# Kernel tuning notes

Hardware: AMD Instinct MI355X
Metric: run time of the kernel (lower is better)

The kernel has to match this reference:

```python
import jax, jax.numpy as jnp
import numpy as np

NUM_MOVIES = 100000
MOVIE_FEAT = 128
USER_FEAT = 128
BATCH = 16384
N_NBRS = 50
D0, D1, D2 = 256, 256, 128  # layer_dims


def setup_inputs() -> dict:
    key = jax.random.key(0)
    ks = jax.random.split(key, 16)
    inp = {
        "users": jax.random.normal(ks[0], (BATCH, USER_FEAT), jnp.float32),
        "pos_movies": jax.random.normal(ks[1], (BATCH, MOVIE_FEAT), jnp.float32),
        "neg_movies": jax.random.normal(ks[2], (BATCH, MOVIE_FEAT), jnp.float32),
        "user_ids": jax.random.randint(ks[3], (BATCH,), 0, BATCH),
        "pos_movie_ids": jax.random.randint(ks[4], (BATCH,), 0, NUM_MOVIES),
        "neg_movie_ids": jax.random.randint(ks[5], (BATCH,), 0, NUM_MOVIES),
        "nbr_ids": jax.random.randint(ks[6], (BATCH, N_NBRS), 0, NUM_MOVIES),
        # learned params / buffers
        "movie_table": jax.random.normal(ks[7], (NUM_MOVIES, MOVIE_FEAT), jnp.float32),
        "Wu": jax.random.normal(ks[8], (USER_FEAT, D0), jnp.float32) * (1.0 / np.sqrt(USER_FEAT)),
        "bu": jnp.zeros((D0,), jnp.float32),
        "Wm": jax.random.normal(ks[9], (MOVIE_FEAT, D0), jnp.float32) * (1.0 / np.sqrt(MOVIE_FEAT)),
        "bm": jnp.zeros((D0,), jnp.float32),
        "W1": jax.random.normal(ks[10], (D0, D1), jnp.float32) * (1.0 / np.sqrt(D0)),
        "b1": jnp.zeros((D1,), jnp.float32),
        "W2": jax.random.normal(ks[11], (D1, D2), jnp.float32) * (1.0 / np.sqrt(D1)),
        "b2": jnp.zeros((D2,), jnp.float32),
    }
    return inp


def reference(users, pos_movies, neg_movies, user_ids, pos_movie_ids, neg_movie_ids,
              nbr_ids, movie_table, Wu, bu, Wm, bm, W1, b1, W2, b2):
    # user_projection / movie_projection
    user_emb = users @ Wu + bu                      # [B, D0]
    movie_emb = movie_table @ Wm + bm               # [N, D0]
    pos_emb = movie_emb[pos_movie_ids]              # [B, D0]
    neg_emb = movie_emb[neg_movie_ids]              # [B, D0]
    # vectorized replacement of the per-user neighbor gather + mean loop
    nbr_mean = jnp.mean(movie_emb[nbr_ids], axis=1)  # [B, N_NBRS, D0] -> [B, D0]
    user_emb = user_emb + nbr_mean
    x = jnp.stack([user_emb, pos_emb, neg_emb], axis=0)  # [3, B, D0]
    x = jax.nn.relu(x @ W1 + b1)
    x = jax.nn.relu(x @ W2 + b2)
    return (x[0], x[1], x[2])
```

## Files before the change

kernel.cpp:

```cpp
#include <hip/hip_runtime.h>
#include <hip/hip_bf16.h>

#define BATCH_N   16384
#define FEAT      128
#define NNBR      50
#define NUM_MOVIES_N 100000

typedef short  short8  __attribute__((ext_vector_type(8)));
typedef float  floatx4 __attribute__((ext_vector_type(4)));
typedef unsigned int u32;

__device__ __forceinline__ __hip_bfloat16 f2bf(float x) { return __float2bfloat16(x); }
__device__ __forceinline__ float bfb2f(short s) {
  union { u32 u; float f; } c; c.u = ((u32)(unsigned short)s) << 16; return c.f;
}

__device__ __forceinline__ void gld16(const __hip_bfloat16* g, __hip_bfloat16* l) {
  __builtin_amdgcn_global_load_lds(
      (const __attribute__((address_space(1))) u32*)g,
      (__attribute__((address_space(3))) u32*)l, 16, 0, 0);
}

__device__ __forceinline__ floatx4 mfma16(short8 a, short8 b, floatx4 c) {
  return __builtin_amdgcn_mfma_f32_16x16x32_bf16(a, b, c, 0, 0, 0);
}

#define WAITVM2 asm volatile("s_waitcnt vmcnt(2)" ::: "memory")
#define WAITVM0 asm volatile("s_waitcnt vmcnt(0)" ::: "memory")

#define CONV_BLOCKS (NUM_MOVIES_N * FEAT / (256 * 8))
__global__ __launch_bounds__(256) void prep_all(
    const float* __restrict__ t, __hip_bfloat16* __restrict__ tb,
    const float* __restrict__ Wu, const float* __restrict__ Wm,
    const float* __restrict__ W1, const float* __restrict__ W2,
    const float* __restrict__ bu, const float* __restrict__ bm,
    __hip_bfloat16* __restrict__ WcatT, __hip_bfloat16* __restrict__ WmT,
    __hip_bfloat16* __restrict__ W1T,  __hip_bfloat16* __restrict__ W2T,
    float* __restrict__ bc, unsigned int* __restrict__ ctr) {
  int bid = blockIdx.x;
  if (bid < CONV_BLOCKS) {
    size_t i = ((size_t)bid * 256 + threadIdx.x) * 8;
    float4 v0 = *(const float4*)(t + i);
    float4 v1 = *(const float4*)(t + i + 4);
    __hip_bfloat16 o[8];
    o[0] = f2bf(v0.x); o[1] = f2bf(v0.y); o[2] = f2bf(v0.z); o[3] = f2bf(v0.w);
    o[4] = f2bf(v1.x); o[5] = f2bf(v1.y); o[6] = f2bf(v1.z); o[7] = f2bf(v1.w);
    *(short8*)(tb + i) = *(short8*)o;
  } else {
    int idx = (bid - CONV_BLOCKS) * 256 + threadIdx.x;
    int n = idx & 255, k = idx >> 8;
    float v = (k < 128) ? Wu[k * 256 + n] : Wm[(k - 128) * 256 + n];
    WcatT[n * 256 + k] = f2bf(v);
    W1T[n * 256 + k]   = f2bf(W1[k * 256 + n]);
    if (k < 128) WmT[n * 128 + k] = f2bf(Wm[k * 256 + n]);
    if (idx < 32768) {
      int k2 = idx >> 7, n2 = idx & 127;
      W2T[n2 * 256 + k2] = f2bf(W2[k2 * 128 + n2]);
    }
    if (idx < 256) bc[idx] = bu[idx] + bm[idx];
    if (idx == 0) *ctr = 0;
  }
}

template <int K0, int NCOL, bool RELU, bool TOGLB>
__device__ __forceinline__ void layer(
    const __hip_bfloat16* Ain,
    const __hip_bfloat16* __restrict__ Wt, const float* __restrict__ bias,
    __hip_bfloat16* Olds, float* __restrict__ Oglb,
    int wid, int quad, int lrow) {
  constexpr int KK = K0 / 32;
  constexpr int JN = NCOL / 128;
  const int c0 = wid * JN * 16;

  short8 bfr[JN][KK];
  float  bv[JN];
  #pragma unroll
  for (int j = 0; j < JN; ++j) {
    #pragma unroll
    for (int kc = 0; kc < KK; ++kc)
      bfr[j][kc] = *(const short8*)(Wt + (size_t)(c0 + j * 16 + lrow) * K0 +
                                    kc * 32 + quad * 8);
    bv[j] = bias[c0 + j * 16 + lrow];
  }

  #pragma unroll
  for (int it = 0; it < 4; ++it) {
    int r = it * 16 + lrow;
    short8 af[KK];
    #pragma unroll
    for (int kc = 0; kc < KK; ++kc)
      af[kc] = *(const short8*)&Ain[r * K0 + (((kc * 4 + quad) ^ (r & 7)) << 3)];
    floatx4 pa[JN], pb[JN];
    #pragma unroll
    for (int j = 0; j < JN; ++j) { pa[j] = {}; pb[j] = {}; }
    #pragma unroll
    for (int kc = 0; kc < KK; kc += 2)
      #pragma unroll
      for (int j = 0; j < JN; ++j) {
        pa[j] = mfma16(af[kc],     bfr[j][kc],     pa[j]);
        pb[j] = mfma16(af[kc + 1], bfr[j][kc + 1], pb[j]);
      }
    #pragma unroll
    for (int j = 0; j < JN; ++j) {
      floatx4 a = pa[j] + pb[j];
      int col = c0 + j * 16 + lrow;
      #pragma unroll
      for (int rr = 0; rr < 4; ++rr) {
        int row = it * 16 + quad * 4 + rr;
        float v = a[rr] + bv[j];
        if (RELU) v = fmaxf(v, 0.f);
        if (TOGLB) {
          Oglb[(size_t)row * NCOL + col] = v;
        } else {
          int ch = col >> 3;
          Olds[row * 256 + (((ch ^ (row & 7)) << 3) | (col & 7))] = f2bf(v);
        }
      }
    }
  }
}

__global__ __launch_bounds__(512)
__attribute__((amdgpu_waves_per_eu(2, 2)))
void fused_mlp(
    const float* __restrict__ users,
    const __hip_bfloat16* __restrict__ tb,
    const int* __restrict__ pos_ids, const int* __restrict__ neg_ids,
    const int* __restrict__ nbr_ids,
    const __hip_bfloat16* __restrict__ WcatT,
    const __hip_bfloat16* __restrict__ WmT,
    const __hip_bfloat16* __restrict__ W1T,
    const __hip_bfloat16* __restrict__ W2T,
    const float* __restrict__ bc, const float* __restrict__ bmv,
    const float* __restrict__ b1, const float* __restrict__ b2,
    __hip_bfloat16* __restrict__ A_user, unsigned int* __restrict__ ctr,
    float* __restrict__ out) {
  __shared__ __hip_bfloat16 A_lds[64 * 256];
  __shared__ __hip_bfloat16 E_lds[64 * 256];

  const int t    = threadIdx.x;
  const int lane = t & 63, wid = t >> 6;
  const int quad = lane >> 4, lrow = lane & 15;
  const int b    = blockIdx.x;

  if (b < 256) {
    const long m0 = (long)b * 64;
    const int rbase = wid << 3;
    const int* nbw = nbr_ids + (size_t)(m0 + rbase) * NNBR;
    int idreg[7];
    #pragma unroll
    for (int w = 0; w < 7; ++w) {
      int fl = w * 64 + lane;
      idreg[w] = nbw[fl < 8 * NNBR ? fl : 8 * NNBR - 1];
    }
    __hip_bfloat16* stg = E_lds + (wid << 11);

    auto getid = [&](int fb) -> int {
      int idx = fb + quad;
      int v = __shfl(idreg[fb >> 6], idx & 63, 64);
      if ((fb >> 6) != ((fb + 3) >> 6)) {
        int v2 = __shfl(idreg[(fb + 3) >> 6], idx & 63, 64);
        v = ((idx >> 6) == (fb >> 6)) ? v : v2;
      }
      return v;
    };
    auto issue = [&](int k) {
      int row = k / 7, c = k % 7;
      int id0 = getid(row * NNBR + c * 8);
      int id1 = getid(row * NNBR + c * 8 + 4);
      __hip_bfloat16* dst = stg + ((k & 1) << 10);
      gld16(tb + (size_t)id0 * FEAT + (lrow << 3), dst + (lane << 3));
      gld16(tb + (size_t)id1 * FEAT + (lrow << 3), dst + 512 + (lane << 3));
    };

    issue(0); issue(1);
    float acc[8] = {0.f, 0.f, 0.f, 0.f, 0.f, 0.f, 0.f, 0.f};
    #pragma unroll
    for (int k = 0; k < 56; ++k) {
      if (k < 55) { WAITVM2; } else { WAITVM0; }
      const __hip_bfloat16* bb = stg + ((k & 1) << 10);
      int c = k % 7;
      short8 x0 = *(const short8*)(bb + (lane << 3));
      if (c < 6) {
        short8 x1 = *(const short8*)(bb + 512 + (lane << 3));
        #pragma unroll
        for (int e = 0; e < 8; ++e) { acc[e] += bfb2f(x0[e]); acc[e] += bfb2f(x1[e]); }
      } else if (quad < 2) {
        #pragma unroll
        for (int e = 0; e < 8; ++e) acc[e] += bfb2f(x0[e]);
      }
      if (c == 6) {
        int row = k / 7;
        __hip_bfloat16 o[8];
        #pragma unroll
        for (int e = 0; e < 8; ++e) {
          float v = acc[e];
          v += __shfl_xor(v, 16, 64);
          v += __shfl_xor(v, 32, 64);
          o[e] = f2bf(v * (1.f / NNBR));
          acc[e] = 0.f;
        }
        if (quad == 0)
          *(short8*)(A_user + (size_t)(m0 + rbase + row) * 128 + (lrow << 3)) =
              *(short8*)o;
      }
      __builtin_amdgcn_sched_barrier(0);
      if (k + 2 < 56) issue(k + 2);
    }
    WAITVM0;
    __syncthreads();
    if (t == 0)
      __hip_atomic_fetch_add(ctr, 1u, __ATOMIC_RELEASE, __HIP_MEMORY_SCOPE_AGENT);
    return;
  }

  if (b < 768) {
    int k = b - 256;
    const int s = 1 + (k & 1);
    const long m0 = (long)(k >> 1) * 64;
    const int* ids = (s == 1) ? pos_ids : neg_ids;
    #pragma unroll
    for (int i = 0; i < 2; ++i) {
      int c = t + i * 512;
      int r = c >> 4, sl = c & 15;
      int id = ids[m0 + r];
      gld16(tb + ((size_t)id << 7) + ((sl ^ (r & 7)) << 3),
            A_lds + (c << 3));
    }
    __syncthreads();

    layer<128, 256, false, false>(A_lds, WmT, bmv, E_lds, nullptr,
                                  wid, quad, lrow);
    __syncthreads();
    layer<256, 256, true, false>(E_lds, W1T, b1, A_lds, nullptr,
                                 wid, quad, lrow);
    __syncthreads();
    layer<256, 128, true, true>(A_lds, W2T, b2, nullptr,
                                out + ((size_t)s * BATCH_N + m0) * 128,
                                wid, quad, lrow);
    return;
  }

  {
    const long m0 = (long)(b - 768) * 64;
    if (t == 0) {
      while (__hip_atomic_load(ctr, __ATOMIC_ACQUIRE, __HIP_MEMORY_SCOPE_AGENT)
             < 256u)
        __builtin_amdgcn_s_sleep(8);
    }
    __syncthreads();

    const int rbase = wid << 3;
    for (int rr = 0; rr < 8; ++rr) {
      const int r = rbase | rr;
      const size_t grow = (size_t)(m0 + r);
      if (quad == 0) {
        short8 m = *(const short8*)(A_user + grow * 128 + (lrow << 3));
        int ch = 16 + lrow;
        *(short8*)(A_lds + r * 256 + ((ch ^ (r & 7)) << 3)) = m;
      }
      float2 uv = ((const float2*)(users + grow * FEAT))[lane];
      __hip_bfloat162 t0; t0.x = f2bf(uv.x); t0.y = f2bf(uv.y);
      int col = lane << 1, ch2 = col >> 3;
      *(__hip_bfloat162*)(A_lds + r * 256 + ((ch2 ^ (r & 7)) << 3) + (col & 7)) = t0;
    }
    __syncthreads();

    layer<256, 256, false, false>(A_lds, WcatT, bc, E_lds, nullptr,
                                  wid, quad, lrow);
    __syncthreads();
    layer<256, 256, true, false>(E_lds, W1T, b1, A_lds, nullptr,
                                 wid, quad, lrow);
    __syncthreads();
    layer<256, 128, true, true>(A_lds, W2T, b2, nullptr,
                                out + (size_t)m0 * 128,
                                wid, quad, lrow);
  }
}

extern "C" void kernel_launch(void* const* d_in, const int* in_sizes, int n_in,
                              void* d_out, int out_size, void* d_ws, size_t ws_size,
                              hipStream_t stream) {
  const float* users   = (const float*)d_in[0];
  const int*   pos_ids = (const int*)d_in[4];
  const int*   neg_ids = (const int*)d_in[5];
  const int*   nbr_ids = (const int*)d_in[6];
  const float* table   = (const float*)d_in[7];
  const float* Wu = (const float*)d_in[8];
  const float* bu = (const float*)d_in[9];
  const float* Wm = (const float*)d_in[10];
  const float* bm = (const float*)d_in[11];
  const float* W1 = (const float*)d_in[12];
  const float* b1 = (const float*)d_in[13];
  const float* W2 = (const float*)d_in[14];
  const float* b2 = (const float*)d_in[15];
  float* out = (float*)d_out;

  char* p = (char*)d_ws;
  auto carve = [&](size_t bytes) { char* r = p; p += (bytes + 255) & ~(size_t)255; return r; };
  __hip_bfloat16* tb     = (__hip_bfloat16*)carve((size_t)NUM_MOVIES_N * FEAT * 2);
  __hip_bfloat16* WcatT  = (__hip_bfloat16*)carve(256 * 256 * 2);
  __hip_bfloat16* WmT    = (__hip_bfloat16*)carve(256 * 128 * 2);
  __hip_bfloat16* W1T    = (__hip_bfloat16*)carve(256 * 256 * 2);
  __hip_bfloat16* W2T    = (__hip_bfloat16*)carve(128 * 256 * 2);
  float*          bc     = (float*)carve(256 * 4);
  __hip_bfloat16* A_user = (__hip_bfloat16*)carve((size_t)BATCH_N * 128 * 2);
  unsigned int*   ctr    = (unsigned int*)carve(256);

  prep_all<<<CONV_BLOCKS + 256, 256, 0, stream>>>(
      table, tb, Wu, Wm, W1, W2, bu, bm, WcatT, WmT, W1T, W2T, bc, ctr);
  fused_mlp<<<1024, 512, 0, stream>>>(
      users, tb, pos_ids, neg_ids, nbr_ids, WcatT, WmT, W1T, W2T,
      bc, bm, b1, b2, A_user, ctr, out);
}
```

Before: 209.2 us.

## Fuse user MLP into neighbor-gather blocks and deepen gather prefetch to four stages

The 256 neighbor-mean blocks now run the user-side three-layer MLP themselves, right after writing their averaged rows. This removes the separate user blocks, the global atomic counter and the spin-wait, so the grid drops from 1024 to 768 blocks. The gather pipeline also goes from a double buffer to a four-deep ring that uses all of LDS as staging, keeping more gathers in flight. The trade-off is that each user block now does gather and MLP in sequence, which may leave CUs less balanced, and the averaged rows still make a round trip through global memory.

```diff
diff --git a/kernel.cpp b/kernel.cpp
--- a/kernel.cpp
+++ b/kernel.cpp
@@ -25,6 +25,8 @@
   return __builtin_amdgcn_mfma_f32_16x16x32_bf16(a, b, c, 0, 0, 0);
 }
 
+#define WAITVM6 asm volatile("s_waitcnt vmcnt(6)" ::: "memory")
+#define WAITVM4 asm volatile("s_waitcnt vmcnt(4)" ::: "memory")
 #define WAITVM2 asm volatile("s_waitcnt vmcnt(2)" ::: "memory")
 #define WAITVM0 asm volatile("s_waitcnt vmcnt(0)" ::: "memory")
 
@@ -36,7 +38,7 @@
     const float* __restrict__ bu, const float* __restrict__ bm,
     __hip_bfloat16* __restrict__ WcatT, __hip_bfloat16* __restrict__ WmT,
     __hip_bfloat16* __restrict__ W1T,  __hip_bfloat16* __restrict__ W2T,
-    float* __restrict__ bc, unsigned int* __restrict__ ctr) {
+    float* __restrict__ bc) {
   int bid = blockIdx.x;
   if (bid < CONV_BLOCKS) {
     size_t i = ((size_t)bid * 256 + threadIdx.x) * 8;
@@ -58,7 +60,6 @@
       W2T[n2 * 256 + k2] = f2bf(W2[k2 * 128 + n2]);
     }
     if (idx < 256) bc[idx] = bu[idx] + bm[idx];
-    if (idx == 0) *ctr = 0;
   }
 }
 
@@ -133,11 +134,11 @@
     const __hip_bfloat16* __restrict__ W2T,
     const float* __restrict__ bc, const float* __restrict__ bmv,
     const float* __restrict__ b1, const float* __restrict__ b2,
-    __hip_bfloat16* __restrict__ A_user, unsigned int* __restrict__ ctr,
+    __hip_bfloat16* __restrict__ A_user,
     float* __restrict__ out) {
-  __shared__ __hip_bfloat16 A_lds[64 * 256];
-  __shared__ __hip_bfloat16 E_lds[64 * 256];
-
+  __shared__ __hip_bfloat16 LDS[64 * 512];
+  __hip_bfloat16* A_lds = LDS;
+  __hip_bfloat16* E_lds = LDS + 64 * 256;
   const int t    = threadIdx.x;
   const int lane = t & 63, wid = t >> 6;
   const int quad = lane >> 4, lrow = lane & 15;
@@ -153,7 +154,7 @@
       int fl = w * 64 + lane;
       idreg[w] = nbw[fl < 8 * NNBR ? fl : 8 * NNBR - 1];
     }
-    __hip_bfloat16* stg = E_lds + (wid << 11);
+    __hip_bfloat16* stg = LDS + (wid << 12);
 
     auto getid = [&](int fb) -> int {
       int idx = fb + quad;
@@ -168,17 +169,20 @@
       int row = k / 7, c = k % 7;
       int id0 = getid(row * NNBR + c * 8);
       int id1 = getid(row * NNBR + c * 8 + 4);
-      __hip_bfloat16* dst = stg + ((k & 1) << 10);
+      __hip_bfloat16* dst = stg + ((k & 3) << 10);
       gld16(tb + (size_t)id0 * FEAT + (lrow << 3), dst + (lane << 3));
       gld16(tb + (size_t)id1 * FEAT + (lrow << 3), dst + 512 + (lane << 3));
     };
 
-    issue(0); issue(1);
+    issue(0); issue(1); issue(2); issue(3);
     float acc[8] = {0.f, 0.f, 0.f, 0.f, 0.f, 0.f, 0.f, 0.f};
     #pragma unroll
     for (int k = 0; k < 56; ++k) {
-      if (k < 55) { WAITVM2; } else { WAITVM0; }
-      const __hip_bfloat16* bb = stg + ((k & 1) << 10);
+      if (k <= 52)      { WAITVM6; }
+      else if (k == 53) { WAITVM4; }
+      else if (k == 54) { WAITVM2; }
+      else              { WAITVM0; }
+      const __hip_bfloat16* bb = stg + ((k & 3) << 10);
       int c = k % 7;
       short8 x0 = *(const short8*)(bb + (lane << 3));
       if (c < 6) {
@@ -205,52 +209,11 @@
               *(short8*)o;
       }
       __builtin_amdgcn_sched_barrier(0);
-      if (k + 2 < 56) issue(k + 2);
+      if (k + 4 < 56) issue(k + 4);
     }
     WAITVM0;
     __syncthreads();
-    if (t == 0)
-      __hip_atomic_fetch_add(ctr, 1u, __ATOMIC_RELEASE, __HIP_MEMORY_SCOPE_AGENT);
-    return;
-  }
-
-  if (b < 768) {
-    int k = b - 256;
-    const int s = 1 + (k & 1);
-    const long m0 = (long)(k >> 1) * 64;
-    const int* ids = (s == 1) ? pos_ids : neg_ids;
-    #pragma unroll
-    for (int i = 0; i < 2; ++i) {
-      int c = t + i * 512;
-      int r = c >> 4, sl = c & 15;
-      int id = ids[m0 + r];
-      gld16(tb + ((size_t)id << 7) + ((sl ^ (r & 7)) << 3),
-            A_lds + (c << 3));
-    }
-    __syncthreads();
-
-    layer<128, 256, false, false>(A_lds, WmT, bmv, E_lds, nullptr,
-                                  wid, quad, lrow);
-    __syncthreads();
-    layer<256, 256, true, false>(E_lds, W1T, b1, A_lds, nullptr,
-                                 wid, quad, lrow);
-    __syncthreads();
-    layer<256, 128, true, true>(A_lds, W2T, b2, nullptr,
-                                out + ((size_t)s * BATCH_N + m0) * 128,
-                                wid, quad, lrow);
-    return;
-  }
-
-  {
-    const long m0 = (long)(b - 768) * 64;
-    if (t == 0) {
-      while (__hip_atomic_load(ctr, __ATOMIC_ACQUIRE, __HIP_MEMORY_SCOPE_AGENT)
-             < 256u)
-        __builtin_amdgcn_s_sleep(8);
-    }
-    __syncthreads();
-
-    const int rbase = wid << 3;
+
     for (int rr = 0; rr < 8; ++rr) {
       const int r = rbase | rr;
       const size_t grow = (size_t)(m0 + r);
@@ -274,6 +237,33 @@
     __syncthreads();
     layer<256, 128, true, true>(A_lds, W2T, b2, nullptr,
                                 out + (size_t)m0 * 128,
+                                wid, quad, lrow);
+    return;
+  }
+
+  {
+    int k = b - 256;
+    const int s = 1 + (k & 1);
+    const long m0 = (long)(k >> 1) * 64;
+    const int* ids = (s == 1) ? pos_ids : neg_ids;
+    #pragma unroll
+    for (int i = 0; i < 2; ++i) {
+      int c = t + i * 512;
+      int r = c >> 4, sl = c & 15;
+      int id = ids[m0 + r];
+      gld16(tb + ((size_t)id << 7) + ((sl ^ (r & 7)) << 3),
+            A_lds + (c << 3));
+    }
+    __syncthreads();
+
+    layer<128, 256, false, false>(A_lds, WmT, bmv, E_lds, nullptr,
+                                  wid, quad, lrow);
+    __syncthreads();
+    layer<256, 256, true, false>(E_lds, W1T, b1, A_lds, nullptr,
+                                 wid, quad, lrow);
+    __syncthreads();
+    layer<256, 128, true, true>(A_lds, W2T, b2, nullptr,
+                                out + ((size_t)s * BATCH_N + m0) * 128,
                                 wid, quad, lrow);
   }
 }
@@ -305,11 +295,10 @@
   __hip_bfloat16* W2T    = (__hip_bfloat16*)carve(128 * 256 * 2);
   float*          bc     = (float*)carve(256 * 4);
   __hip_bfloat16* A_user = (__hip_bfloat16*)carve((size_t)BATCH_N * 128 * 2);
-  unsigned int*   ctr    = (unsigned int*)carve(256);
 
   prep_all<<<CONV_BLOCKS + 256, 256, 0, stream>>>(
-      table, tb, Wu, Wm, W1, W2, bu, bm, WcatT, WmT, W1T, W2T, bc, ctr);
-  fused_mlp<<<1024, 512, 0, stream>>>(
+      table, tb, Wu, Wm, W1, W2, bu, bm, WcatT, WmT, W1T, W2T, bc);
+  fused_mlp<<<768, 512, 0, stream>>>(
       users, tb, pos_ids, neg_ids, nbr_ids, WcatT, WmT, W1T, W2T,
-      bc, bm, b1, b2, A_user, ctr, out);
-}
+      bc, bm, b1, b2, A_user, out);
+}
```

After: 203.7 us. 1.03x faster.
